# Optimization experiments

Hardware: AMD Instinct MI355X
Metric: run time of the kernel (lower is better)

## Reference

```python
import jax, jax.numpy as jnp
import numpy as np

DIM = 1024
NUM_HEADS = 16
DH = DIM // NUM_HEADS  # 64
B, S = 4, 2048


def setup_inputs() -> dict:
    key = jax.random.key(0)
    ks = jax.random.split(key, 9)
    sc = 0.02
    x = jax.random.normal(ks[0], (B, S, DIM), dtype=jnp.float32)
    # per-head projection weights stacked: [H, DIM, DH] (input-major layout)
    Wq = jax.random.normal(ks[1], (NUM_HEADS, DIM, DH), dtype=jnp.float32) * sc
    Wk = jax.random.normal(ks[2], (NUM_HEADS, DIM, DH), dtype=jnp.float32) * sc
    Wv = jax.random.normal(ks[3], (NUM_HEADS, DIM, DH), dtype=jnp.float32) * sc
    bq = jax.random.normal(ks[4], (NUM_HEADS, DH), dtype=jnp.float32) * sc
    bk = jax.random.normal(ks[5], (NUM_HEADS, DH), dtype=jnp.float32) * sc
    bv = jax.random.normal(ks[6], (NUM_HEADS, DH), dtype=jnp.float32) * sc
    Wo = jax.random.normal(ks[7], (DIM, DIM), dtype=jnp.float32) * sc  # (in, out)
    bo = jax.random.normal(ks[8], (DIM,), dtype=jnp.float32) * sc
    return {"x": x, "Wq": Wq, "Wk": Wk, "Wv": Wv,
            "bq": bq, "bk": bk, "bv": bv, "Wo": Wo, "bo": bo}


def reference(x, Wq, Wk, Wv, bq, bk, bv, Wo, bo):
    # Per-head Linear projections, vectorized over heads: [B,H,S,DH]
    q = jnp.einsum('bsd,hde->bhse', x, Wq) + bq[None, :, None, :]
    k = jnp.einsum('bsd,hde->bhse', x, Wk) + bk[None, :, None, :]
    v = jnp.einsum('bsd,hde->bhse', x, Wv) + bv[None, :, None, :]
    # attention_matmul: Q @ K^T normalized by sqrt(dim_per_head)
    scale = 1.0 / jnp.sqrt(jnp.asarray(DH, dtype=x.dtype))
    scores = jnp.einsum('bhse,bhte->bhst', q, k) * scale  # [B,H,S,S]
    attn = jax.nn.softmax(scores, axis=-1)
    # attn_drop with p=0.0 is identity
    o = jnp.einsum('bhst,bhte->bhse', attn, v)  # [B,H,S,DH]
    # concat along last dim in head order -> [B,S,H*DH]
    o = jnp.transpose(o, (0, 2, 1, 3)).reshape(x.shape[0], x.shape[1], NUM_HEADS * DH)
    # output projection (proj_drop p=0.0 is identity)
    return o @ Wo + bo
```

## Files before the change

### kernel.cpp

```cpp
#include <hip/hip_runtime.h>
#include <stdint.h>

#define DIM 1024
#define NH 16
#define DH 64
#define BATCH 4
#define SEQ 2048
#define MROWS (BATCH*SEQ)

typedef _Float16 half8 __attribute__((ext_vector_type(8)));
typedef __fp16 fp16x2 __attribute__((ext_vector_type(2)));
typedef float f32x4 __attribute__((ext_vector_type(4)));
typedef float f32x16 __attribute__((ext_vector_type(16)));
typedef unsigned int u32x2 __attribute__((ext_vector_type(2)));

__device__ __forceinline__ unsigned short f2h(float f) {
    union { _Float16 h; unsigned short u; } c; c.h = (_Float16)f; return c.u;
}
__device__ __forceinline__ unsigned int pk2u(float a, float b) {
    union { fp16x2 h; unsigned int u; } c;
    c.h = __builtin_amdgcn_cvt_pkrtz(a, b);
    return c.u;
}
__device__ __forceinline__ float fexp2(float x) {
    return __builtin_amdgcn_exp2f(x);
}
__device__ __forceinline__ void gl_lds16(const unsigned short* g, unsigned short* l) {
    __builtin_amdgcn_global_load_lds(
        (__attribute__((address_space(1))) void*)(void*)g,
        (__attribute__((address_space(3))) void*)(void*)l,
        16, 0, 0);
}


__global__ void cast_x_kernel(const float* __restrict__ x,
                              unsigned short* __restrict__ xh, int n4) {
    int i = blockIdx.x * blockDim.x + threadIdx.x;
    if (i >= n4) return;
    float4 v = reinterpret_cast<const float4*>(x)[i];
    uint2 o;
    o.x = pk2u(v.x, v.y);
    o.y = pk2u(v.z, v.w);
    reinterpret_cast<uint2*>(xh)[i] = o;
}

__global__ __launch_bounds__(256) void prep_wqkv_kernel(
    const float* __restrict__ Wq, const float* __restrict__ Wk,
    const float* __restrict__ Wv, unsigned short* __restrict__ wt)
{
    __shared__ unsigned short tile[64][65];
    const int d0 = blockIdx.x * 64;
    const int h = blockIdx.y;
    const int mat = blockIdx.z;
    const float* W = (mat == 0) ? Wq : ((mat == 1) ? Wk : Wv);
    const int c = threadIdx.x & 63;
    const int rr = threadIdx.x >> 6;
#pragma unroll
    for (int p = 0; p < 16; p++) {
        int dl = p * 4 + rr;
        tile[dl][c] = f2h(W[((size_t)h * 1024 + d0 + dl) * 64 + c]);
    }
    __syncthreads();
#pragma unroll
    for (int p = 0; p < 16; p++) {
        int el = p * 4 + rr;
        wt[(((size_t)(mat * NH + h) * 64) + el) * DIM + d0 + c] = tile[c][el];
    }
}

__global__ __launch_bounds__(256) void prep_wo_kernel(
    const float* __restrict__ Wo, unsigned short* __restrict__ wot)
{
    __shared__ unsigned short tile[64][65];
    const int d0 = blockIdx.x * 64;
    const int o0 = blockIdx.y * 64;
    const int c = threadIdx.x & 63;
    const int rr = threadIdx.x >> 6;
#pragma unroll
    for (int p = 0; p < 16; p++) {
        int dl = p * 4 + rr;
        tile[dl][c] = f2h(Wo[(size_t)(d0 + dl) * DIM + o0 + c]);
    }
    __syncthreads();
#pragma unroll
    for (int p = 0; p < 16; p++) {
        int ol = p * 4 + rr;
        wot[(size_t)(o0 + ol) * DIM + d0 + c] = tile[c][ol];
    }
}

__global__ __launch_bounds__(256) void transpose_v_kernel(
    const unsigned short* __restrict__ Vb, unsigned short* __restrict__ Vt)
{
    __shared__ unsigned short tile[64][65];
    const int s0 = blockIdx.x * 64;
    const size_t bh = (size_t)blockIdx.z * NH + blockIdx.y;
    const int c = threadIdx.x & 63;
    const int rr = threadIdx.x >> 6;
    const unsigned short* src = Vb + bh * SEQ * DH;
    unsigned short* dst = Vt + bh * DH * SEQ;
#pragma unroll
    for (int p = 0; p < 16; p++) {
        int sl = p * 4 + rr;
        tile[sl][c] = src[(size_t)(s0 + sl) * DH + c];
    }
    __syncthreads();
#pragma unroll
    for (int p = 0; p < 16; p++) {
        int dr = p * 4 + rr;
        dst[(size_t)dr * SEQ + s0 + c] = tile[c][dr];
    }
}

__global__ __launch_bounds__(256) void qkv_gemm_kernel(
    const unsigned short* __restrict__ xh,
    const unsigned short* __restrict__ wt,
    const float* __restrict__ bq, const float* __restrict__ bk,
    const float* __restrict__ bv,
    unsigned short* __restrict__ Qb,
    unsigned short* __restrict__ Kb,
    unsigned short* __restrict__ Vb)
{
    const int rowblk = blockIdx.x;
    const int hpair = blockIdx.y;
    const int mat = blockIdx.z;
    const int wave = threadIdx.x >> 6;
    const int lane = threadIdx.x & 63;
    const int quad = lane >> 4;
    const int lr = lane & 15;
    const int mhalf = wave & 1;
    const int nhalf = wave >> 1;

    __shared__ __align__(16) unsigned short Ab[2][128 * 32];
    __shared__ __align__(16) unsigned short Bt[2][128 * 32];

    const unsigned short* Asrc = xh + (size_t)rowblk * 128 * DIM;
    const unsigned short* Bsrc = wt + (size_t)(mat * NH + hpair * 2) * DH * DIM;

    const int srow = lane >> 2;
    const int scs = lane & 3;

    f32x4 acc[4][4];
#pragma unroll
    for (int mt = 0; mt < 4; mt++)
#pragma unroll
        for (int nt = 0; nt < 4; nt++) acc[mt][nt] = (f32x4){0.f, 0.f, 0.f, 0.f};

    auto stage = [&](int k0, int sel) {
#pragma unroll
        for (int jj = 0; jj < 2; jj++) {
            const int j = wave * 2 + jj;
            const int r = j * 16 + srow;
            const int cg = scs ^ ((r >> 1) & 3);
            gl_lds16(Asrc + (size_t)r * DIM + k0 + cg * 8, &Ab[sel][j * 512]);
            gl_lds16(Bsrc + (size_t)r * DIM + k0 + cg * 8, &Bt[sel][j * 512]);
        }
    };

    stage(0, 0);
    __syncthreads();

    for (int i = 0; i < DIM / 32; i++) {
        const int sel = i & 1;
        if (i + 1 < DIM / 32) stage((i + 1) * 32, sel ^ 1);

        half8 af[4], bf[4];
#pragma unroll
        for (int mt = 0; mt < 4; mt++) {
            const int row = mhalf * 64 + mt * 16 + lr;
            const int slot = quad ^ ((row >> 1) & 3);
            af[mt] = *reinterpret_cast<const half8*>(&Ab[sel][row * 32 + slot * 8]);
        }
#pragma unroll
        for (int nt = 0; nt < 4; nt++) {
            const int row = nhalf * 64 + nt * 16 + lr;
            const int slot = quad ^ ((row >> 1) & 3);
            bf[nt] = *reinterpret_cast<const half8*>(&Bt[sel][row * 32 + slot * 8]);
        }
#pragma unroll
        for (int mt = 0; mt < 4; mt++)
#pragma unroll
            for (int nt = 0; nt < 4; nt++)
                acc[mt][nt] = __builtin_amdgcn_mfma_f32_16x16x32_f16(
                    af[mt], bf[nt], acc[mt][nt], 0, 0, 0);
        __syncthreads();
    }

    const float* bias = (mat == 0) ? bq : ((mat == 1) ? bk : bv);
    const float scale = (mat == 0) ? 0.1803368801111601f : 1.0f;
    unsigned short* outp = (mat == 0) ? Qb : ((mat == 1) ? Kb : Vb);
    const int rowBase = rowblk * 128 + mhalf * 64;
    const int bb = rowBase / SEQ;
    const int sBase = rowBase % SEQ;

#pragma unroll
    for (int mt = 0; mt < 4; mt++) {
        const int s0 = sBase + mt * 16 + quad * 4;
#pragma unroll
        for (int nt = 0; nt < 4; nt++) {
            const int e = nhalf * 64 + nt * 16 + lr;
            const int head = hpair * 2 + (e >> 6);
            const int n = e & 63;
            const float bvl = bias[head * DH + n];
            const size_t base = (size_t)(bb * NH + head) * SEQ * DH;
#pragma unroll
            for (int r = 0; r < 4; r++) {
                outp[base + (size_t)(s0 + r) * DH + n] = f2h((acc[mt][nt][r] + bvl) * scale);
            }
        }
    }
}

__global__ __launch_bounds__(256, 4) void attn_kernel(
    const unsigned short* __restrict__ Qb,
    const unsigned short* __restrict__ Kb,
    const unsigned short* __restrict__ Vt,
    unsigned short* __restrict__ Ob)
{
    const int h = blockIdx.y;
    const int bb = blockIdx.z;
    const int wave = threadIdx.x >> 6;
    const int lane = threadIdx.x & 63;
    const int ql = lane & 31;
    const int hi = lane >> 5;
    const int qBase = blockIdx.x * 128 + wave * 32;

    const size_t bh = (size_t)(bb * NH + h);
    const unsigned short* Qh = Qb + bh * SEQ * DH;
    const unsigned short* Kh = Kb + bh * SEQ * DH;
    const unsigned short* Vh = Vt + bh * DH * SEQ;

    __shared__ __align__(16) unsigned short Kbuf[2][64 * 64];
    __shared__ __align__(16) unsigned short Vbuf[2][64 * 64];

    const int srow = lane >> 3;
    const int scs = lane & 7;
    int koff[2], voff[2];
#pragma unroll
    for (int jj = 0; jj < 2; jj++) {
        const int r = wave * 16 + jj * 8 + srow;
        const int cg = scs ^ srow ^ ((wave * 2 + jj) & 3);
        koff[jj] = r * DH + cg * 8;
        voff[jj] = r * SEQ + cg * 8;
    }

    auto stage_k = [&](int kt, int sel) {
        const size_t base = (size_t)kt * 64 * DH;
        gl_lds16(Kh + base + koff[0], &Kbuf[sel][wave * 1024]);
        gl_lds16(Kh + base + koff[1], &Kbuf[sel][wave * 1024 + 512]);
    };
    auto stage_v = [&](int kt, int sel) {
        const size_t base = (size_t)kt * 64;
        gl_lds16(Vh + base + voff[0], &Vbuf[sel][wave * 1024]);
        gl_lds16(Vh + base + voff[1], &Vbuf[sel][wave * 1024 + 512]);
    };

    half8 qf[4];
#pragma unroll
    for (int ks = 0; ks < 4; ks++)
        qf[ks] = *reinterpret_cast<const half8*>(
            Qh + (size_t)(qBase + ql) * DH + ks * 16 + hi * 8);

    const int slotx = (ql & 7) ^ ((ql >> 3) & 3);
    int rowb[2], soff[4];
#pragma unroll
    for (int b = 0; b < 2; b++) rowb[b] = (b * 32 + ql) * 64;
#pragma unroll
    for (int ks = 0; ks < 4; ks++) soff[ks] = ((ks * 2 + hi) ^ slotx) * 8;

    f32x16 z16;
#pragma unroll
    for (int e = 0; e < 16; e++) z16[e] = 0.f;

    f32x16 o[2];
#pragma unroll
    for (int mt = 0; mt < 2; mt++) o[mt] = z16;
    float lsA = 0.f, lsB = 0.f;
    half8 pf[4];

    auto burst = [&](int sel, bool doPV) {
        f32x16 sacc[2];
        __builtin_amdgcn_s_setprio(1);
#pragma unroll
        for (int ks = 0; ks < 4; ks++) {
#pragma unroll
            for (int b = 0; b < 2; b++) {
                half8 kf = *reinterpret_cast<const half8*>(
                    &Kbuf[sel][rowb[b] + soff[ks]]);
                sacc[b] = __builtin_amdgcn_mfma_f32_32x32x16_f16(
                    kf, qf[ks], ks ? sacc[b] : z16, 0, 0, 0);
            }
            if (doPV) {
#pragma unroll
                for (int mt = 0; mt < 2; mt++) {
                    half8 vf = *reinterpret_cast<const half8*>(
                        &Vbuf[sel][rowb[mt] + soff[ks]]);
                    o[mt] = __builtin_amdgcn_mfma_f32_32x32x16_f16(
                        vf, pf[ks], o[mt], 0, 0, 0);
                }
            }
        }
        __builtin_amdgcn_s_setprio(0);

#pragma unroll
        for (int kb = 0; kb < 2; kb++) {
            unsigned int c[8];
#pragma unroll
            for (int m = 0; m < 8; m++) {
                float a = fexp2(sacc[kb][2 * m]);
                float b2 = fexp2(sacc[kb][2 * m + 1]);
                if (m & 1) lsB += a + b2; else lsA += a + b2;
                c[m] = pk2u(a, b2);
            }
#pragma unroll
            for (int ks = 0; ks < 2; ks++) {
                u32x2 w02 = __builtin_amdgcn_permlane32_swap(
                    c[4 * ks + 0], c[4 * ks + 2], false, false);
                u32x2 w13 = __builtin_amdgcn_permlane32_swap(
                    c[4 * ks + 1], c[4 * ks + 3], false, false);
                union { unsigned int u[4]; half8 h; } cv;
                cv.u[0] = w02[0]; cv.u[1] = w13[0];
                cv.u[2] = w02[1]; cv.u[3] = w13[1];
                pf[kb * 2 + ks] = cv.h;
            }
        }
    };

    stage_k(0, 0);
    __syncthreads();

    stage_k(1, 1);
    stage_v(0, 1);
    burst(0, false);
    __syncthreads();

    for (int i = 1; i < SEQ / 64; i++) {
        const int sel = i & 1;
        if (i + 1 < SEQ / 64) stage_k(i + 1, sel ^ 1);
        stage_v(i, sel ^ 1);
        burst(sel, true);
        __syncthreads();
    }

    __builtin_amdgcn_s_setprio(1);
#pragma unroll
    for (int ks = 0; ks < 4; ks++)
#pragma unroll
        for (int mt = 0; mt < 2; mt++) {
            half8 vf = *reinterpret_cast<const half8*>(
                &Vbuf[0][rowb[mt] + soff[ks]]);
            o[mt] = __builtin_amdgcn_mfma_f32_32x32x16_f16(
                vf, pf[ks], o[mt], 0, 0, 0);
        }
    __builtin_amdgcn_s_setprio(0);

    float l = lsA + lsB;
    l += __shfl_xor(l, 32);
    const float inv = 1.f / l;
    const size_t orow = (size_t)(bb * SEQ + qBase + ql) * DIM + h * DH;
#pragma unroll
    for (int mt = 0; mt < 2; mt++) {
#pragma unroll
        for (int g = 0; g < 4; g++) {
            uint2 pkd;
            pkd.x = pk2u(o[mt][4 * g + 0] * inv, o[mt][4 * g + 1] * inv);
            pkd.y = pk2u(o[mt][4 * g + 2] * inv, o[mt][4 * g + 3] * inv);
            *reinterpret_cast<uint2*>(Ob + orow + mt * 32 + 8 * g + 4 * hi) = pkd;
        }
    }
}

__global__ __launch_bounds__(256) void out_proj_kernel(
    const unsigned short* __restrict__ Ob,
    const unsigned short* __restrict__ wot,
    const float* __restrict__ bo,
    float* __restrict__ out)
{
    const int rowblk = blockIdx.x;
    const int colblk = blockIdx.y;
    const int wave = threadIdx.x >> 6;
    const int lane = threadIdx.x & 63;
    const int quad = lane >> 4;
    const int lr = lane & 15;
    const int mhalf = wave & 1;
    const int nhalf = wave >> 1;

    __shared__ __align__(16) unsigned short Ab[2][128 * 32];
    __shared__ __align__(16) unsigned short Bt[2][128 * 32];

    const unsigned short* Asrc = Ob + (size_t)rowblk * 128 * DIM;
    const unsigned short* Bsrc = wot + (size_t)colblk * 128 * DIM;

    const int srow = lane >> 2;
    const int scs = lane & 3;

    f32x4 acc[4][4];
#pragma unroll
    for (int mt = 0; mt < 4; mt++)
#pragma unroll
        for (int nt = 0; nt < 4; nt++) acc[mt][nt] = (f32x4){0.f, 0.f, 0.f, 0.f};

    auto stage = [&](int k0, int sel) {
#pragma unroll
        for (int jj = 0; jj < 2; jj++) {
            const int j = wave * 2 + jj;
            const int r = j * 16 + srow;
            const int cg = scs ^ ((r >> 1) & 3);
            gl_lds16(Asrc + (size_t)r * DIM + k0 + cg * 8, &Ab[sel][j * 512]);
            gl_lds16(Bsrc + (size_t)r * DIM + k0 + cg * 8, &Bt[sel][j * 512]);
        }
    };

    stage(0, 0);
    __syncthreads();

    for (int i = 0; i < DIM / 32; i++) {
        const int sel = i & 1;
        if (i + 1 < DIM / 32) stage((i + 1) * 32, sel ^ 1);

        half8 af[4], bf[4];
#pragma unroll
        for (int mt = 0; mt < 4; mt++) {
            const int row = mhalf * 64 + mt * 16 + lr;
            const int slot = quad ^ ((row >> 1) & 3);
            af[mt] = *reinterpret_cast<const half8*>(&Ab[sel][row * 32 + slot * 8]);
        }
#pragma unroll
        for (int nt = 0; nt < 4; nt++) {
            const int row = nhalf * 64 + nt * 16 + lr;
            const int slot = quad ^ ((row >> 1) & 3);
            bf[nt] = *reinterpret_cast<const half8*>(&Bt[sel][row * 32 + slot * 8]);
        }
#pragma unroll
        for (int mt = 0; mt < 4; mt++)
#pragma unroll
            for (int nt = 0; nt < 4; nt++)
                acc[mt][nt] = __builtin_amdgcn_mfma_f32_16x16x32_f16(
                    af[mt], bf[nt], acc[mt][nt], 0, 0, 0);
        __syncthreads();
    }

    const int rowBase = rowblk * 128 + mhalf * 64;
    const int colBase = colblk * 128 + nhalf * 64;
#pragma unroll
    for (int mt = 0; mt < 4; mt++) {
#pragma unroll
        for (int nt = 0; nt < 4; nt++) {
            const int col = colBase + nt * 16 + lr;
            const float bias = bo[col];
#pragma unroll
            for (int r = 0; r < 4; r++) {
                int row = rowBase + mt * 16 + quad * 4 + r;
                out[(size_t)row * DIM + col] = acc[mt][nt][r] + bias;
            }
        }
    }
}


extern "C" void kernel_launch(void* const* d_in, const int* in_sizes, int n_in,
                              void* d_out, int out_size, void* d_ws, size_t ws_size,
                              hipStream_t stream) {
    const float* x  = (const float*)d_in[0];
    const float* Wq = (const float*)d_in[1];
    const float* Wk = (const float*)d_in[2];
    const float* Wv = (const float*)d_in[3];
    const float* bq = (const float*)d_in[4];
    const float* bk = (const float*)d_in[5];
    const float* bv = (const float*)d_in[6];
    const float* Wo = (const float*)d_in[7];
    const float* bo = (const float*)d_in[8];
    float* out = (float*)d_out;

    unsigned short* xh  = (unsigned short*)d_ws;
    unsigned short* wt  = xh  + (size_t)MROWS * DIM;
    unsigned short* wot = wt  + (size_t)3 * NH * DH * DIM;
    unsigned short* Qb  = wot + (size_t)DIM * DIM;
    unsigned short* Kb  = Qb  + (size_t)BATCH * NH * SEQ * DH;
    unsigned short* Vb  = Kb  + (size_t)BATCH * NH * SEQ * DH;
    unsigned short* Vt  = Vb  + (size_t)BATCH * NH * SEQ * DH;
    unsigned short* Ob  = Vt  + (size_t)BATCH * NH * SEQ * DH;

    {
        int n4 = MROWS * DIM / 4;
        cast_x_kernel<<<(n4 + 255) / 256, 256, 0, stream>>>(x, xh, n4);
    }
    prep_wqkv_kernel<<<dim3(16, NH, 3), 256, 0, stream>>>(Wq, Wk, Wv, wt);
    prep_wo_kernel<<<dim3(16, 16), 256, 0, stream>>>(Wo, wot);
    qkv_gemm_kernel<<<dim3(64, 8, 3), 256, 0, stream>>>(xh, wt, bq, bk, bv, Qb, Kb, Vb);
    transpose_v_kernel<<<dim3(SEQ / 64, NH, BATCH), 256, 0, stream>>>(Vb, Vt);
    attn_kernel<<<dim3(SEQ / 128, NH, BATCH), 256, 0, stream>>>(Qb, Kb, Vt, Ob);
    out_proj_kernel<<<dim3(64, 8), 256, 0, stream>>>(Ob, wot, bo, out);
}
```

Baseline: 310.3 us.

## Replace double-buffered K/V staging with triple-buffer ring and vmcnt waits

The attention kernel's K and V tiles now live in a three-slot shared-memory ring instead of two buffers. K is prefetched two tiles ahead and V one tile ahead. Each iteration waits only for the previous iteration's global-to-LDS loads (partial vmcnt) and then issues one raw barrier, which removes the extra full synchronisation. The prologue is simplified and the Q fragment load is hoisted. The trade-off is more LDS per block (48 KB instead of 32 KB), which may cut the number of resident blocks per CU.

```diff
diff --git a/kernel.cpp b/kernel.cpp
--- a/kernel.cpp
+++ b/kernel.cpp
@@ -224,14 +224,21 @@
     const int ql = lane & 31;
     const int hi = lane >> 5;
     const int qBase = blockIdx.x * 128 + wave * 32;
+    const int NT = SEQ / 64;
 
     const size_t bh = (size_t)(bb * NH + h);
     const unsigned short* Qh = Qb + bh * SEQ * DH;
     const unsigned short* Kh = Kb + bh * SEQ * DH;
     const unsigned short* Vh = Vt + bh * DH * SEQ;
 
-    __shared__ __align__(16) unsigned short Kbuf[2][64 * 64];
-    __shared__ __align__(16) unsigned short Vbuf[2][64 * 64];
+    __shared__ __align__(16) unsigned short Kring[3][64 * 64];
+    __shared__ __align__(16) unsigned short Vring[3][64 * 64];
+
+    half8 qf[4];
+#pragma unroll
+    for (int ks = 0; ks < 4; ks++)
+        qf[ks] = *reinterpret_cast<const half8*>(
+            Qh + (size_t)(qBase + ql) * DH + ks * 16 + hi * 8);
 
     const int srow = lane >> 3;
     const int scs = lane & 7;
@@ -244,22 +251,16 @@
         voff[jj] = r * SEQ + cg * 8;
     }
 
-    auto stage_k = [&](int kt, int sel) {
+    auto stage_k = [&](int kt, int dst) {
         const size_t base = (size_t)kt * 64 * DH;
-        gl_lds16(Kh + base + koff[0], &Kbuf[sel][wave * 1024]);
-        gl_lds16(Kh + base + koff[1], &Kbuf[sel][wave * 1024 + 512]);
+        gl_lds16(Kh + base + koff[0], &Kring[dst][wave * 1024]);
+        gl_lds16(Kh + base + koff[1], &Kring[dst][wave * 1024 + 512]);
     };
-    auto stage_v = [&](int kt, int sel) {
+    auto stage_v = [&](int kt, int dst) {
         const size_t base = (size_t)kt * 64;
-        gl_lds16(Vh + base + voff[0], &Vbuf[sel][wave * 1024]);
-        gl_lds16(Vh + base + voff[1], &Vbuf[sel][wave * 1024 + 512]);
+        gl_lds16(Vh + base + voff[0], &Vring[dst][wave * 1024]);
+        gl_lds16(Vh + base + voff[1], &Vring[dst][wave * 1024 + 512]);
     };
-
-    half8 qf[4];
-#pragma unroll
-    for (int ks = 0; ks < 4; ks++)
-        qf[ks] = *reinterpret_cast<const half8*>(
-            Qh + (size_t)(qBase + ql) * DH + ks * 16 + hi * 8);
 
     const int slotx = (ql & 7) ^ ((ql >> 3) & 3);
     int rowb[2], soff[4];
@@ -278,7 +279,7 @@
     float lsA = 0.f, lsB = 0.f;
     half8 pf[4];
 
-    auto burst = [&](int sel, bool doPV) {
+    auto burst = [&](int ksel, int vsel, bool doPV) {
         f32x16 sacc[2];
         __builtin_amdgcn_s_setprio(1);
 #pragma unroll
@@ -286,7 +287,7 @@
 #pragma unroll
             for (int b = 0; b < 2; b++) {
                 half8 kf = *reinterpret_cast<const half8*>(
-                    &Kbuf[sel][rowb[b] + soff[ks]]);
+                    &Kring[ksel][rowb[b] + soff[ks]]);
                 sacc[b] = __builtin_amdgcn_mfma_f32_32x32x16_f16(
                     kf, qf[ks], ks ? sacc[b] : z16, 0, 0, 0);
             }
@@ -294,7 +295,7 @@
 #pragma unroll
                 for (int mt = 0; mt < 2; mt++) {
                     half8 vf = *reinterpret_cast<const half8*>(
-                        &Vbuf[sel][rowb[mt] + soff[ks]]);
+                        &Vring[vsel][rowb[mt] + soff[ks]]);
                     o[mt] = __builtin_amdgcn_mfma_f32_32x32x16_f16(
                         vf, pf[ks], o[mt], 0, 0, 0);
                 }
@@ -327,28 +328,34 @@
     };
 
     stage_k(0, 0);
-    __syncthreads();
-
     stage_k(1, 1);
-    stage_v(0, 1);
-    burst(0, false);
-    __syncthreads();
-
-    for (int i = 1; i < SEQ / 64; i++) {
-        const int sel = i & 1;
-        if (i + 1 < SEQ / 64) stage_k(i + 1, sel ^ 1);
-        stage_v(i, sel ^ 1);
-        burst(sel, true);
-        __syncthreads();
-    }
-
+    stage_v(0, 0);
+
+    for (int i = 0; i < NT; i++) {
+        asm volatile("s_waitcnt vmcnt(4)" ::: "memory");
+        __builtin_amdgcn_sched_barrier(0);
+        __builtin_amdgcn_s_barrier();
+        __builtin_amdgcn_sched_barrier(0);
+
+        const int k2 = (i + 2 < NT) ? i + 2 : NT - 1;
+        const int v1 = (i + 1 < NT) ? i + 1 : NT - 1;
+        stage_k(k2, (i + 2) % 3);
+        stage_v(v1, (i + 1) % 3);
+
+        burst(i % 3, (i + 2) % 3 , i > 0);
+    }
+
+    asm volatile("s_waitcnt vmcnt(0)" ::: "memory");
+    __builtin_amdgcn_sched_barrier(0);
+    __builtin_amdgcn_s_barrier();
+    __builtin_amdgcn_sched_barrier(0);
     __builtin_amdgcn_s_setprio(1);
 #pragma unroll
     for (int ks = 0; ks < 4; ks++)
 #pragma unroll
         for (int mt = 0; mt < 2; mt++) {
             half8 vf = *reinterpret_cast<const half8*>(
-                &Vbuf[0][rowb[mt] + soff[ks]]);
+                &Vring[(SEQ / 64 - 1) % 3][rowb[mt] + soff[ks]]);
             o[mt] = __builtin_amdgcn_mfma_f32_32x32x16_f16(
                 vf, pf[ks], o[mt], 0, 0, 0);
         }
```

Measured after the change: 328.1 us. 5.7% more time.

## Split attention KV range across two wave groups and read V directly from global

Applied to the files above, without the earlier changes.

The attention block grows to 512 threads so that two groups of four waves each process half of the key sequence for the same query tile. The partial outputs and row sums are combined through LDS at the end. V fragments are now loaded straight from global memory instead of being staged in LDS, and the PV MFMA moves after the softmax inside each step rather than being software-pipelined one step behind. This doubles the waves per query tile to raise latency hiding, at the cost of uncached-in-LDS V loads, an extra reduction with a block barrier, and the loss of the previous QK/PV overlap.

```diff
diff --git a/kernel.cpp b/kernel.cpp
--- a/kernel.cpp
+++ b/kernel.cpp
@@ -211,7 +211,7 @@
     }
 }
 
-__global__ __launch_bounds__(256, 4) void attn_kernel(
+__global__ __launch_bounds__(512, 6) void attn_kernel(
     const unsigned short* __restrict__ Qb,
     const unsigned short* __restrict__ Kb,
     const unsigned short* __restrict__ Vt,
@@ -219,41 +219,23 @@
 {
     const int h = blockIdx.y;
     const int bb = blockIdx.z;
-    const int wave = threadIdx.x >> 6;
+    const int w = threadIdx.x >> 6;
+    const int half = w >> 2;
+    const int qt = w & 3;
     const int lane = threadIdx.x & 63;
     const int ql = lane & 31;
     const int hi = lane >> 5;
-    const int qBase = blockIdx.x * 128 + wave * 32;
+    const int qBase = blockIdx.x * 128 + qt * 32;
+    const int NTH = SEQ / 64 / 2;
 
     const size_t bh = (size_t)(bb * NH + h);
     const unsigned short* Qh = Qb + bh * SEQ * DH;
     const unsigned short* Kh = Kb + bh * SEQ * DH;
     const unsigned short* Vh = Vt + bh * DH * SEQ;
 
-    __shared__ __align__(16) unsigned short Kbuf[2][64 * 64];
-    __shared__ __align__(16) unsigned short Vbuf[2][64 * 64];
-
-    const int srow = lane >> 3;
-    const int scs = lane & 7;
-    int koff[2], voff[2];
-#pragma unroll
-    for (int jj = 0; jj < 2; jj++) {
-        const int r = wave * 16 + jj * 8 + srow;
-        const int cg = scs ^ srow ^ ((wave * 2 + jj) & 3);
-        koff[jj] = r * DH + cg * 8;
-        voff[jj] = r * SEQ + cg * 8;
-    }
-
-    auto stage_k = [&](int kt, int sel) {
-        const size_t base = (size_t)kt * 64 * DH;
-        gl_lds16(Kh + base + koff[0], &Kbuf[sel][wave * 1024]);
-        gl_lds16(Kh + base + koff[1], &Kbuf[sel][wave * 1024 + 512]);
-    };
-    auto stage_v = [&](int kt, int sel) {
-        const size_t base = (size_t)kt * 64;
-        gl_lds16(Vh + base + voff[0], &Vbuf[sel][wave * 1024]);
-        gl_lds16(Vh + base + voff[1], &Vbuf[sel][wave * 1024 + 512]);
-    };
+    __shared__ __align__(16) unsigned short Kbuf[2][2][64 * 64];
+    __shared__ float lred[4][32];
+    float* Obuf = reinterpret_cast<float*>(&Kbuf[0][0][0]);
 
     half8 qf[4];
 #pragma unroll
@@ -261,6 +243,22 @@
         qf[ks] = *reinterpret_cast<const half8*>(
             Qh + (size_t)(qBase + ql) * DH + ks * 16 + hi * 8);
 
+    const int srow = lane >> 3;
+    const int scs = lane & 7;
+    int koff[2];
+#pragma unroll
+    for (int jj = 0; jj < 2; jj++) {
+        const int r = qt * 16 + jj * 8 + srow;
+        const int cg = scs ^ srow ^ ((qt * 2 + jj) & 3);
+        koff[jj] = r * DH + cg * 8;
+    }
+
+    auto stage_k = [&](int i, int sel) {
+        const size_t base = (size_t)(half * NTH + i) * 64 * DH;
+        gl_lds16(Kh + base + koff[0], &Kbuf[half][sel][qt * 1024]);
+        gl_lds16(Kh + base + koff[1], &Kbuf[half][sel][qt * 1024 + 512]);
+    };
+
     const int slotx = (ql & 7) ^ ((ql >> 3) & 3);
     int rowb[2], soff[4];
 #pragma unroll
@@ -268,6 +266,11 @@
 #pragma unroll
     for (int ks = 0; ks < 4; ks++) soff[ks] = ((ks * 2 + hi) ^ slotx) * 8;
 
+    const unsigned short* Vrow[2];
+#pragma unroll
+    for (int mt = 0; mt < 2; mt++)
+        Vrow[mt] = Vh + (size_t)(mt * 32 + ql) * SEQ + hi * 8;
+
     f32x16 z16;
 #pragma unroll
     for (int e = 0; e < 16; e++) z16[e] = 0.f;
@@ -276,9 +279,8 @@
 #pragma unroll
     for (int mt = 0; mt < 2; mt++) o[mt] = z16;
     float lsA = 0.f, lsB = 0.f;
-    half8 pf[4];
-
-    auto burst = [&](int sel, bool doPV) {
+
+    auto compute = [&](int i, int sel) {
         f32x16 sacc[2];
         __builtin_amdgcn_s_setprio(1);
 #pragma unroll
@@ -286,22 +288,14 @@
 #pragma unroll
             for (int b = 0; b < 2; b++) {
                 half8 kf = *reinterpret_cast<const half8*>(
-                    &Kbuf[sel][rowb[b] + soff[ks]]);
+                    &Kbuf[half][sel][rowb[b] + soff[ks]]);
                 sacc[b] = __builtin_amdgcn_mfma_f32_32x32x16_f16(
                     kf, qf[ks], ks ? sacc[b] : z16, 0, 0, 0);
             }
-            if (doPV) {
-#pragma unroll
-                for (int mt = 0; mt < 2; mt++) {
-                    half8 vf = *reinterpret_cast<const half8*>(
-                        &Vbuf[sel][rowb[mt] + soff[ks]]);
-                    o[mt] = __builtin_amdgcn_mfma_f32_32x32x16_f16(
-                        vf, pf[ks], o[mt], 0, 0, 0);
-                }
-            }
         }
         __builtin_amdgcn_s_setprio(0);
 
+        half8 pf[4];
 #pragma unroll
         for (int kb = 0; kb < 2; kb++) {
             unsigned int c[8];
@@ -318,54 +312,71 @@
                     c[4 * ks + 0], c[4 * ks + 2], false, false);
                 u32x2 w13 = __builtin_amdgcn_permlane32_swap(
                     c[4 * ks + 1], c[4 * ks + 3], false, false);
-                union { unsigned int u[4]; half8 h; } cv;
+                union { unsigned int u[4]; half8 hh; } cv;
                 cv.u[0] = w02[0]; cv.u[1] = w13[0];
                 cv.u[2] = w02[1]; cv.u[3] = w13[1];
-                pf[kb * 2 + ks] = cv.h;
-            }
-        }
+                pf[kb * 2 + ks] = cv.hh;
+            }
+        }
+
+        const int kcol = (half * NTH + i) * 64;
+        __builtin_amdgcn_s_setprio(1);
+#pragma unroll
+        for (int ks = 0; ks < 4; ks++) {
+#pragma unroll
+            for (int mt = 0; mt < 2; mt++) {
+                half8 vf = *reinterpret_cast<const half8*>(
+                    Vrow[mt] + kcol + ks * 16);
+                o[mt] = __builtin_amdgcn_mfma_f32_32x32x16_f16(
+                    vf, pf[ks], o[mt], 0, 0, 0);
+            }
+        }
+        __builtin_amdgcn_s_setprio(0);
     };
 
     stage_k(0, 0);
     __syncthreads();
 
-    stage_k(1, 1);
-    stage_v(0, 1);
-    burst(0, false);
-    __syncthreads();
-
-    for (int i = 1; i < SEQ / 64; i++) {
+    for (int i = 0; i < NTH; i++) {
         const int sel = i & 1;
-        if (i + 1 < SEQ / 64) stage_k(i + 1, sel ^ 1);
-        stage_v(i, sel ^ 1);
-        burst(sel, true);
+        if (i + 1 < NTH) stage_k(i + 1, sel ^ 1);
+        compute(i, sel);
         __syncthreads();
     }
-
-    __builtin_amdgcn_s_setprio(1);
-#pragma unroll
-    for (int ks = 0; ks < 4; ks++)
-#pragma unroll
-        for (int mt = 0; mt < 2; mt++) {
-            half8 vf = *reinterpret_cast<const half8*>(
-                &Vbuf[0][rowb[mt] + soff[ks]]);
-            o[mt] = __builtin_amdgcn_mfma_f32_32x32x16_f16(
-                vf, pf[ks], o[mt], 0, 0, 0);
-        }
-    __builtin_amdgcn_s_setprio(0);
 
     float l = lsA + lsB;
     l += __shfl_xor(l, 32);
-    const float inv = 1.f / l;
-    const size_t orow = (size_t)(bb * SEQ + qBase + ql) * DIM + h * DH;
-#pragma unroll
-    for (int mt = 0; mt < 2; mt++) {
-#pragma unroll
-        for (int g = 0; g < 4; g++) {
-            uint2 pkd;
-            pkd.x = pk2u(o[mt][4 * g + 0] * inv, o[mt][4 * g + 1] * inv);
-            pkd.y = pk2u(o[mt][4 * g + 2] * inv, o[mt][4 * g + 3] * inv);
-            *reinterpret_cast<uint2*>(Ob + orow + mt * 32 + 8 * g + 4 * hi) = pkd;
+
+    if (half == 1) {
+#pragma unroll
+        for (int mt = 0; mt < 2; mt++)
+#pragma unroll
+            for (int g = 0; g < 4; g++)
+#pragma unroll
+                for (int rr = 0; rr < 4; rr++) {
+                    const int dh = mt * 32 + 8 * g + 4 * hi + rr;
+                    Obuf[(qt * 64 + dh) * 32 + ql] = o[mt][4 * g + rr];
+                }
+        if (lane < 32) lred[qt][lane] = l;
+    }
+    __syncthreads();
+    if (half == 0) {
+        const float inv = 1.f / (l + lred[qt][ql]);
+        const size_t orow = (size_t)(bb * SEQ + qBase + ql) * DIM + h * DH;
+#pragma unroll
+        for (int mt = 0; mt < 2; mt++) {
+#pragma unroll
+            for (int g = 0; g < 4; g++) {
+                const int dh0 = mt * 32 + 8 * g + 4 * hi;
+                float s0 = o[mt][4 * g + 0] + Obuf[(qt * 64 + dh0 + 0) * 32 + ql];
+                float s1 = o[mt][4 * g + 1] + Obuf[(qt * 64 + dh0 + 1) * 32 + ql];
+                float s2 = o[mt][4 * g + 2] + Obuf[(qt * 64 + dh0 + 2) * 32 + ql];
+                float s3 = o[mt][4 * g + 3] + Obuf[(qt * 64 + dh0 + 3) * 32 + ql];
+                uint2 pkd;
+                pkd.x = pk2u(s0 * inv, s1 * inv);
+                pkd.y = pk2u(s2 * inv, s3 * inv);
+                *reinterpret_cast<uint2*>(Ob + orow + dh0) = pkd;
+            }
         }
     }
 }
@@ -489,6 +500,6 @@
     prep_wo_kernel<<<dim3(16, 16), 256, 0, stream>>>(Wo, wot);
     qkv_gemm_kernel<<<dim3(64, 8, 3), 256, 0, stream>>>(xh, wt, bq, bk, bv, Qb, Kb, Vb);
     transpose_v_kernel<<<dim3(SEQ / 64, NH, BATCH), 256, 0, stream>>>(Vb, Vt);
-    attn_kernel<<<dim3(SEQ / 128, NH, BATCH), 256, 0, stream>>>(Qb, Kb, Vt, Ob);
+    attn_kernel<<<dim3(SEQ / 128, NH, BATCH), 512, 0, stream>>>(Qb, Kb, Vt, Ob);
     out_proj_kernel<<<dim3(64, 8), 256, 0, stream>>>(Ob, wot, bo, out);
 }
```

Measured after the change: 551.0 us. 1.78x slower.
